# Kernel tuning notes

Measured on AMD Instinct MI355X. Metric: run time of the kernel, lower is better.

The kernel has to match this reference:

```python
import jax, jax.numpy as jnp
import numpy as np
from jax import lax

K = 8            # number of object slots
H = 250          # hidden / fc_size
EPS = 1e-5
DN = ('NCHW', 'OIHW', 'NCHW')


def ln_all(x):
    # F.layer_norm over all non-batch dims, no affine params (torch init: w=1,b=0)
    ax = tuple(range(1, x.ndim))
    m = jnp.mean(x, ax, keepdims=True)
    v = jnp.var(x, ax, keepdims=True)
    return (x - m) * lax.rsqrt(v + EPS)


def ln_last(x):
    # nn.LayerNorm(feat) -> last dim only
    m = jnp.mean(x, -1, keepdims=True)
    v = jnp.var(x, -1, keepdims=True)
    return (x - m) * lax.rsqrt(v + EPS)


def conv(x, w, b):
    # torch Conv2d(k=4, s=2, p=1), NCHW
    y = lax.conv_general_dilated(x, w, (2, 2), [(1, 1), (1, 1)], dimension_numbers=DN)
    return y + b[None, :, None, None]


def up4(x):
    return jnp.repeat(jnp.repeat(x, 4, axis=2), 4, axis=3)


def setup_inputs():
    ks = jax.random.split(jax.random.key(0), 20)
    bk = 48 * K
    p = lambda i, shape, s: jax.random.normal(ks[i], shape, jnp.float32) * s
    z = lambda n: jnp.zeros((n,), jnp.float32)
    return dict(
        x=p(0, (bk, 4096), 1.0),
        state=p(1, (bk, H), 1.0),
        # encoder convs (OIHW) + fc
        c1w=p(2, (16, 1, 4, 4), 0.25), c1b=z(16),
        c2w=p(3, (32, 16, 4, 4), 0.06), c2b=z(32),
        c3w=p(4, (64, 32, 4, 4), 0.04), c3b=z(64),
        efc_w=p(5, (4096, 512), 0.016), efc_b=z(512),
        # R_NEM (weights stored as [in, out])
        renc_w=p(6, (H, H), 0.06), renc_b=z(H),
        core_w=p(7, (2 * H, H), 0.045), core_b=z(H),
        ctx_w=p(8, (H, H), 0.06), ctx_b=z(H),
        att1_w=p(9, (H, 100), 0.06), att1_b=z(100),
        att2_w=p(10, (100, 1), 0.1), att2_b=z(1),
        out_w=p(11, (2 * H + 512, H), 0.03), out_b=z(H),
        # decoder fcs + convs
        dfc1_w=p(12, (H, 512), 0.06), dfc1_b=z(512),
        dfc2_w=p(13, (512, 4096), 0.045), dfc2_b=z(4096),
        d1w=p(14, (32, 64, 4, 4), 0.03), d1b=z(32),
        d2w=p(15, (16, 32, 4, 4), 0.045), d2b=z(16),
        d3w=p(16, (1, 16, 4, 4), 0.06), d3b=z(1),
    )


def reference(x, state, c1w, c1b, c2w, c2b, c3w, c3b, efc_w, efc_b,
              renc_w, renc_b, core_w, core_b, ctx_w, ctx_b,
              att1_w, att1_b, att2_w, att2_b, out_w, out_b,
              dfc1_w, dfc1_b, dfc2_w, dfc2_b, d1w, d1b, d2w, d2b, d3w, d3b):
    bk = x.shape[0]
    b = bk // K

    # ---------------- EncoderLayer ----------------
    def inwrap(h, w, bias):  # InputWrapper conv branch: NHWC -> permute(0,3,2,1) -> conv -> back
        y = conv(jnp.transpose(h, (0, 3, 2, 1)), w, bias)
        return jax.nn.elu(ln_all(jnp.transpose(y, (0, 3, 2, 1))))

    h = x.reshape(bk, 64, 64, 1)
    h = inwrap(h, c1w, c1b)                 # (bk,32,32,16)
    h = inwrap(h, c2w, c2b)                 # (bk,16,16,32)
    h = inwrap(h, c3w, c3b)                 # (bk,8,8,64)
    h = h.reshape(bk, -1)                   # (bk,4096)
    h = jax.nn.elu(ln_last(h @ efc_w + efc_b))   # (bk,512)

    # ---------------- R_NEM (RecurrentLayer) ----------------
    s1 = jax.nn.relu(ln_last(state @ renc_w + renc_b))   # (bk,H)
    s1r = s1.reshape(b, K, H)
    idx = np.array([[j for j in range(K) if j != i] for i in range(K)])  # (K,K-1)
    cs = s1r[:, idx, :]                                    # context: (b,K,K-1,H)
    fs = jnp.broadcast_to(s1r[:, :, None, :], cs.shape)    # focus copies
    pair = jnp.concatenate([fs, cs], axis=-1)              # (b,K,K-1,2H)
    core = jax.nn.relu(ln_last(pair @ core_w + core_b))    # (b,K,K-1,H)
    ctx = jax.nn.relu(ln_last(core @ ctx_w + ctx_b))       # (b,K,K-1,H)
    att = jax.nn.sigmoid(jnp.tanh(ln_last(core @ att1_w + att1_b)) @ att2_w + att2_b)  # (b,K,K-1,1)
    effect = jnp.sum(ctx * att, axis=2).reshape(bk, H)     # attention-weighted sum over K-1
    total = jnp.concatenate([s1, effect, h], axis=1)       # (bk, 2H+512)
    new_state = total @ out_w + out_b                      # (bk,H)
    xr = jax.nn.sigmoid(ln_last(new_state))
    state_out = jax.nn.sigmoid(new_state)

    # ---------------- DecoderLayer ----------------
    d = jax.nn.relu(ln_last(xr @ dfc1_w + dfc1_b))         # (bk,512)
    d = jax.nn.relu(ln_last(d @ dfc2_w + dfc2_b))          # (bk,4096)
    d = d.reshape(bk, 8, 8, 64)

    def outwrap(t, w, bias):
        y = conv(up4(jnp.transpose(t, (0, 3, 2, 1))), w, bias)
        return jnp.transpose(y, (0, 3, 2, 1))

    d = jax.nn.relu(ln_all(outwrap(d, d1w, d1b)))          # (bk,16,16,32)
    d = jax.nn.relu(ln_all(outwrap(d, d2w, d2b)))          # (bk,32,32,16)
    d = jax.nn.sigmoid(outwrap(d, d3w, d3b))               # (bk,64,64,1), no LN
    x_out = d.reshape(bk, -1)                              # (bk,4096)
    return x_out, state_out
```

## Files before the change

### kernel.cpp

```cpp
#include <hip/hip_runtime.h>
#include <hip/hip_bf16.h>
#include <math.h>

typedef __attribute__((ext_vector_type(8))) short bf16x8;
typedef __attribute__((ext_vector_type(4))) float f32x4;

__device__ __forceinline__ float eluf(float v){ return v > 0.f ? v : expm1f(v); }
__device__ __forceinline__ float sigf(float v){ return 1.f/(1.f+expf(-v)); }
__device__ __forceinline__ unsigned short f2bf(float f){
  unsigned u = __float_as_uint(f);
  u += 0x7FFFu + ((u >> 16) & 1u);
  return (unsigned short)(u >> 16);
}
__device__ __forceinline__ float bf2f(short s){
  return __uint_as_float(((unsigned)(unsigned short)s) << 16);
}

__device__ __forceinline__ void block_reduce2(float& a, float& b, float* sbuf){
  __syncthreads();
  for (int off = 32; off; off >>= 1){
    a += __shfl_down(a, off);
    b += __shfl_down(b, off);
  }
  int lane = threadIdx.x & 63, w = threadIdx.x >> 6;
  if (lane == 0){ sbuf[2*w] = a; sbuf[2*w+1] = b; }
  __syncthreads();
  if (threadIdx.x == 0){
    int nw = blockDim.x >> 6;
    float sa = 0.f, sb = 0.f;
    for (int i = 0; i < nw; i++){ sa += sbuf[2*i]; sb += sbuf[2*i+1]; }
    sbuf[0] = sa; sbuf[1] = sb;
  }
  __syncthreads();
  a = sbuf[0]; b = sbuf[1];
}

__device__ __forceinline__ float fold_sum(const float* __restrict__ w, int O, int I,
                                          int o, int i, int pa, int pb, int da, int db){
  float s = 0.f;
  for (int kh = 0; kh < 4; kh++){
    bool inh = (pb==0) ? (db==0 ? (kh==0) : (kh>=1)) : (db==0 ? (kh<=2) : (kh==3));
    if (!inh) continue;
    for (int kw = 0; kw < 4; kw++){
      bool inw = (pa==0) ? (da==0 ? (kw==0) : (kw>=1)) : (da==0 ? (kw<=2) : (kw==3));
      if (!inw) continue;
      s += w[((o*I + i)*4 + kh)*4 + kw];
    }
  }
  return s;
}
__device__ __forceinline__ void fold_elem(const float* __restrict__ w, float* __restrict__ CW,
                                          int O, int I, int l){
  int o = l % O; int q = l / O;
  int da = q & 1, db = (q>>1)&1, pa = (q>>2)&1, pb = (q>>3)&1, i = q>>4;
  CW[(((pb*2+pa)*4 + db*2+da)*I + i)*O + o] = fold_sum(w, O, I, o, i, pa, pb, da, db);
}
__device__ __forceinline__ void cvtc2_elem(const float* __restrict__ w, short* __restrict__ D, int l){
  int i = l & 15, t = (l>>4) & 15, o = l>>8;
  D[l] = (short)f2bf(w[(o*16 + i)*16 + t]);
}
__device__ __forceinline__ void cvtc3_elem(const float* __restrict__ w, short* __restrict__ D, int l){
  int i = l & 31, t = (l>>5) & 15, o = l>>9;
  D[l] = (short)f2bf(w[(o*32 + i)*16 + t]);
}
__device__ __forceinline__ void foldd1_elem(const float* __restrict__ w, short* __restrict__ D, int l){
  int i = l & 63, tap = (l>>6)&3, o = (l>>8)&31, ph = l>>13;
  D[l] = (short)f2bf(fold_sum(w, 32, 64, o, i, ph&1, ph>>1, tap&1, tap>>1));
}
__device__ __forceinline__ void foldd2_elem(const float* __restrict__ w, short* __restrict__ D, int l){
  int i = l & 31, tap = (l>>5)&3, o = (l>>7)&15, ph = l>>11;
  D[l] = (short)f2bf(fold_sum(w, 16, 32, o, i, ph&1, ph>>1, tap&1, tap>>1));
}

__global__ __launch_bounds__(256) void prep_combined(
  const float* __restrict__ efc,  short* __restrict__ Defc,
  const float* __restrict__ dfc2, short* __restrict__ Ddfc2,
  const float* __restrict__ outw, short* __restrict__ Dout,
  const float* __restrict__ corew,short* __restrict__ Dcore,
  const float* __restrict__ dfc1, short* __restrict__ Ddfc1,
  const float* __restrict__ renc, short* __restrict__ Drenc,
  const float* __restrict__ ctx,  short* __restrict__ Dctx,
  const float* __restrict__ att1, short* __restrict__ Datt1,
  const float* __restrict__ d3w, float* __restrict__ CWT3,
  const float* __restrict__ c2w, short* __restrict__ BtC2,
  const float* __restrict__ c3w, short* __restrict__ BtC3,
  const float* __restrict__ d1w, short* __restrict__ BD1,
  const float* __restrict__ d2w, short* __restrict__ BD2,
  const float* __restrict__ state, short* __restrict__ SBF,
  short* __restrict__ TOTb)
{
  int bx = blockIdx.x;
  if (bx >= 1192){
    const int F3=256, P2=F3+8192, P3=P2+32768, P4=P3+32768, P5=P4+8192,
              ST=P5+98304, TOTAL=ST+4608;
    for (int l = (bx-1192)*256 + threadIdx.x; l < TOTAL; l += 256*256){
      if (l < F3)      fold_elem(d3w, CWT3, 1, 16, l);
      else if (l < P2) cvtc2_elem(c2w, BtC2, l - F3);
      else if (l < P3) cvtc3_elem(c3w, BtC3, l - P2);
      else if (l < P4) foldd1_elem(d1w, BD1, l - P3);
      else if (l < P5) foldd2_elem(d2w, BD2, l - P4);
      else if (l < ST){
        int q = l - P5;
        int n = q >> 8, k = q & 255;
        SBF[q] = (k < 250) ? (short)f2bf(state[n*250 + k]) : (short)0;
      } else {
        int q = l - ST;
        int row = q / 12, cc = q % 12;
        int col = cc < 6 ? 250 + cc : 506 + (cc - 6);
        TOTb[row*1024 + col] = 0;
      }
    }
    return;
  }
  const float* W; short* D; int K, N, Kp, base, mode = 0;
  if      (bx < 512) { W=efc;  D=Defc;  K=4096; N=512;  Kp=4096; base=0;    }
  else if (bx < 1024){ W=dfc2; D=Ddfc2; K=512;  N=4096; Kp=512;  base=512;  }
  else if (bx < 1088){ W=outw; D=Dout;  K=1012; N=250;  Kp=1024; base=1024; mode=2; }
  else if (bx < 1120){ W=corew;D=Dcore; K=500;  N=250;  Kp=512;  base=1088; mode=1; }
  else if (bx < 1152){ W=dfc1; D=Ddfc1; K=250;  N=512;  Kp=256;  base=1120; }
  else if (bx < 1168){ W=renc; D=Drenc; K=250;  N=250;  Kp=256;  base=1152; }
  else if (bx < 1184){ W=ctx;  D=Dctx;  K=250;  N=250;  Kp=256;  base=1168; }
  else               { W=att1; D=Datt1; K=250;  N=100;  Kp=256;  base=1184; }
  int t = bx - base;
  int tpr = Kp >> 6;
  int tk = t % tpr, tn = t / tpr;
  __shared__ short tile[64][65];
  int c = threadIdx.x & 63, r4 = threadIdx.x >> 6;
  int n0 = tn*64, k0 = tk*64;
  #pragma unroll 4
  for (int p = 0; p < 16; p++){
    int r = r4*16 + p;
    int k = k0 + r, n = n0 + c;
    int ksrc = k; bool valid;
    if (mode == 0) valid = (k < K);
    else if (mode == 1){ valid = (k < 250) || (k >= 256 && k < 506); ksrc = k < 256 ? k : k - 6; }
    else { valid = (k < 250) || (k >= 256 && k < 506) || (k >= 512);
           ksrc = k < 256 ? k : (k < 512 ? k - 6 : k - 12); }
    float v = (valid && n < N) ? W[(size_t)ksrc*N + n] : 0.f;
    tile[c][r] = (short)f2bf(v);
  }
  __syncthreads();
  #pragma unroll 4
  for (int p = 0; p < 16; p++){
    int nn = r4*16 + p;
    int n = n0 + nn;
    if (n < N) D[(size_t)n*Kp + k0 + c] = tile[nn][c];
  }
}

__global__ __launch_bounds__(256) void gemm_mfma(
    const short* __restrict__ Ab, const short* __restrict__ Bt,
    float* __restrict__ P, int M, int N, int Kp, int Kc)
{
  __shared__ __align__(16) short As[64*32];
  __shared__ __align__(16) short Bs[64*32];
  int tid = threadIdx.x;
  int bm = blockIdx.y*64, bn = blockIdx.x*64;
  int kb = blockIdx.z * Kc;
  int kend = kb + Kc;

  int r = tid >> 2, c = tid & 3;
  const short* Arow = Ab + (size_t)(bm + r)*Kp;
  int gn = bn + r;
  bool bval = gn < N;
  const short* Brow = Bt + (size_t)gn*Kp;

  uint4 hA, hB;
  auto load_regs = [&](int k0){
    hA = *(const uint4*)&Arow[k0 + c*8];
    hB = bval ? *(const uint4*)&Brow[k0 + c*8] : make_uint4(0,0,0,0);
  };
  auto write_lds = [&](){
    *(uint4*)&As[r*32 + c*8] = hA;
    *(uint4*)&Bs[r*32 + c*8] = hB;
  };

  int wave = tid >> 6;
  int ln = tid & 15, quad = (tid >> 4) & 3;
  int wr = (wave >> 1) * 32, wc = (wave & 1) * 32;

  f32x4 zero = {0.f, 0.f, 0.f, 0.f};
  f32x4 acc[2][2] = {{zero, zero}, {zero, zero}};

  load_regs(kb);
  write_lds();
  __syncthreads();
  for (int k0 = kb; k0 < kend; k0 += 32){
    int nxt = k0 + 32;
    if (nxt < kend) load_regs(nxt);
    bf16x8 a0 = *(const bf16x8*)&As[(wr +      ln)*32 + quad*8];
    bf16x8 a1 = *(const bf16x8*)&As[(wr + 16 + ln)*32 + quad*8];
    bf16x8 b0 = *(const bf16x8*)&Bs[(wc +      ln)*32 + quad*8];
    bf16x8 b1 = *(const bf16x8*)&Bs[(wc + 16 + ln)*32 + quad*8];
    acc[0][0] = __builtin_amdgcn_mfma_f32_16x16x32_bf16(a0, b0, acc[0][0], 0, 0, 0);
    acc[0][1] = __builtin_amdgcn_mfma_f32_16x16x32_bf16(a0, b1, acc[0][1], 0, 0, 0);
    acc[1][0] = __builtin_amdgcn_mfma_f32_16x16x32_bf16(a1, b0, acc[1][0], 0, 0, 0);
    acc[1][1] = __builtin_amdgcn_mfma_f32_16x16x32_bf16(a1, b1, acc[1][1], 0, 0, 0);
    __syncthreads();
    if (nxt < kend){ write_lds(); __syncthreads(); }
  }

  float* Pout = P + (size_t)blockIdx.z*M*N;
  #pragma unroll
  for (int t = 0; t < 2; t++)
    #pragma unroll
    for (int u = 0; u < 2; u++)
      #pragma unroll
      for (int j = 0; j < 4; j++){
        int row = bm + wr + t*16 + quad*4 + j;
        int col = bn + wc + u*16 + ln;
        if (col < N) Pout[(size_t)row*N + col] = acc[t][u][j];
      }
}

__global__ __launch_bounds__(256) void gemm_conv2g(
    const short* __restrict__ In, const short* __restrict__ Bt,
    short* __restrict__ Out)
{
  __shared__ __align__(16) short As[128*32];
  __shared__ __align__(16) short Bs[32*32];
  int tid = threadIdx.x;
  int bm = blockIdx.x*128;

  int ra = tid >> 1, ca = (tid & 1)*16;
  int gr = bm + ra;
  int n = gr >> 8, pos = gr & 255;
  int oa = pos >> 4, ob = pos & 15;
  const short* ibase = In + (size_t)n*16384;
  int rb = tid >> 2, cb = (tid & 3)*8;
  const short* Brow = Bt + rb*256;
  bool bact = tid < 128;

  uint4 hA0, hA1, hB;
  auto load_regs = [&](int k0){
    #pragma unroll
    for (int h = 0; h < 2; h++){
      int k = k0 + ca + h*8;
      int tap = k >> 4;
      int ai = 2*oa + (tap & 3) - 1, bi = 2*ob + (tap >> 2) - 1;
      bool v = ((unsigned)ai < 32u) && ((unsigned)bi < 32u);
      uint4 tv = v ? *(const uint4*)&ibase[ai*512 + bi*16 + (k & 15)] : make_uint4(0,0,0,0);
      if (h == 0) hA0 = tv; else hA1 = tv;
    }
    if (bact) hB = *(const uint4*)&Brow[k0 + cb];
  };
  auto write_lds = [&](){
    *(uint4*)&As[ra*32 + ca] = hA0;
    *(uint4*)&As[ra*32 + ca + 8] = hA1;
    if (bact) *(uint4*)&Bs[rb*32 + cb] = hB;
  };

  int wave = tid >> 6, ln = tid & 15, quad = (tid >> 4) & 3;
  int wr = wave * 32;

  f32x4 zero = {0.f,0.f,0.f,0.f};
  f32x4 acc[2][2] = {{zero,zero},{zero,zero}};
  load_regs(0); write_lds(); __syncthreads();
  for (int k0 = 0; k0 < 256; k0 += 32){
    int nxt = k0 + 32;
    if (nxt < 256) load_regs(nxt);
    bf16x8 a0 = *(const bf16x8*)&As[(wr +      ln)*32 + quad*8];
    bf16x8 a1 = *(const bf16x8*)&As[(wr + 16 + ln)*32 + quad*8];
    bf16x8 b0 = *(const bf16x8*)&Bs[(     ln)*32 + quad*8];
    bf16x8 b1 = *(const bf16x8*)&Bs[(16 + ln)*32 + quad*8];
    acc[0][0] = __builtin_amdgcn_mfma_f32_16x16x32_bf16(a0, b0, acc[0][0], 0, 0, 0);
    acc[0][1] = __builtin_amdgcn_mfma_f32_16x16x32_bf16(a0, b1, acc[0][1], 0, 0, 0);
    acc[1][0] = __builtin_amdgcn_mfma_f32_16x16x32_bf16(a1, b0, acc[1][0], 0, 0, 0);
    acc[1][1] = __builtin_amdgcn_mfma_f32_16x16x32_bf16(a1, b1, acc[1][1], 0, 0, 0);
    __syncthreads();
    if (nxt < 256){ write_lds(); __syncthreads(); }
  }
  #pragma unroll
  for (int t = 0; t < 2; t++)
    #pragma unroll
    for (int u = 0; u < 2; u++)
      #pragma unroll
      for (int j = 0; j < 4; j++){
        int row = bm + wr + t*16 + quad*4 + j;
        int col = u*16 + ln;
        Out[(size_t)row*32 + col] = (short)f2bf(acc[t][u][j]);
      }
}

__global__ __launch_bounds__(256) void ln_conv2_act(
    short* __restrict__ E, const float* __restrict__ bias)
{
  __shared__ float sbuf[16];
  int n = blockIdx.x, tid = threadIdx.x;
  short* p = E + (size_t)n*8192;
  float vv[32];
  float s = 0.f, s2 = 0.f;
  #pragma unroll
  for (int t = 0; t < 4; t++){
    bf16x8 v8 = *(const bf16x8*)&p[(t*256 + tid)*8];
    #pragma unroll
    for (int j = 0; j < 8; j++){
      int i = (t*256 + tid)*8 + j;
      float v = bf2f(v8[j]) + bias[i & 31];
      vv[t*8+j] = v; s += v; s2 += v*v;
    }
  }
  block_reduce2(s, s2, sbuf);
  float m = s*(1.f/8192.f);
  float rs = rsqrtf(s2*(1.f/8192.f) - m*m + 1e-5f);
  #pragma unroll
  for (int t = 0; t < 4; t++){
    bf16x8 o8;
    #pragma unroll
    for (int j = 0; j < 8; j++)
      o8[j] = (short)f2bf(eluf((vv[t*8+j]-m)*rs));
    *(bf16x8*)&p[(t*256 + tid)*8] = o8;
  }
}

__global__ __launch_bounds__(256) void gemm_conv3g(
    const short* __restrict__ In, const short* __restrict__ Bt,
    float* __restrict__ P)
{
  __shared__ __align__(16) short As[64*32];
  __shared__ __align__(16) short Bs[64*32];
  int tid = threadIdx.x;
  int bm = blockIdx.x*64;

  int r = tid >> 2, c = tid & 3;
  int gr = bm + r;
  int n = gr >> 6, pos = gr & 63;
  int oa = pos >> 3, ob = pos & 7;
  const short* ibase = In + (size_t)n*8192;
  const short* Brow = Bt + r*512;

  uint4 hA, hB;
  auto load_regs = [&](int k0){
    int k = k0 + c*8;
    int tap = k >> 5;
    int ai = 2*oa + (tap & 3) - 1, bi = 2*ob + (tap >> 2) - 1;
    bool v = ((unsigned)ai < 16u) && ((unsigned)bi < 16u);
    hA = v ? *(const uint4*)&ibase[(ai*16 + bi)*32 + (k & 31)] : make_uint4(0,0,0,0);
    hB = *(const uint4*)&Brow[k];
  };
  auto write_lds = [&](){
    *(uint4*)&As[r*32 + c*8] = hA;
    *(uint4*)&Bs[r*32 + c*8] = hB;
  };

  int wave = tid >> 6, ln = tid & 15, quad = (tid >> 4) & 3;
  int wr = (wave >> 1) * 32, wc = (wave & 1) * 32;

  f32x4 zero = {0.f,0.f,0.f,0.f};
  f32x4 acc[2][2] = {{zero,zero},{zero,zero}};
  load_regs(0); write_lds(); __syncthreads();
  for (int k0 = 0; k0 < 512; k0 += 32){
    int nxt = k0 + 32;
    if (nxt < 512) load_regs(nxt);
    bf16x8 a0 = *(const bf16x8*)&As[(wr +      ln)*32 + quad*8];
    bf16x8 a1 = *(const bf16x8*)&As[(wr + 16 + ln)*32 + quad*8];
    bf16x8 b0 = *(const bf16x8*)&Bs[(wc +      ln)*32 + quad*8];
    bf16x8 b1 = *(const bf16x8*)&Bs[(wc + 16 + ln)*32 + quad*8];
    acc[0][0] = __builtin_amdgcn_mfma_f32_16x16x32_bf16(a0, b0, acc[0][0], 0, 0, 0);
    acc[0][1] = __builtin_amdgcn_mfma_f32_16x16x32_bf16(a0, b1, acc[0][1], 0, 0, 0);
    acc[1][0] = __builtin_amdgcn_mfma_f32_16x16x32_bf16(a1, b0, acc[1][0], 0, 0, 0);
    acc[1][1] = __builtin_amdgcn_mfma_f32_16x16x32_bf16(a1, b1, acc[1][1], 0, 0, 0);
    __syncthreads();
    if (nxt < 512){ write_lds(); __syncthreads(); }
  }
  #pragma unroll
  for (int t = 0; t < 2; t++)
    #pragma unroll
    for (int u = 0; u < 2; u++)
      #pragma unroll
      for (int j = 0; j < 4; j++){
        int row = bm + wr + t*16 + quad*4 + j;
        int col = wc + u*16 + ln;
        P[(size_t)row*64 + col] = acc[t][u][j];
      }
}

__global__ __launch_bounds__(256) void gemm_core_mfma(
    const short* __restrict__ Tb, const short* __restrict__ Bt,
    float* __restrict__ P, int M, int N, int Kc)
{
  __shared__ __align__(16) short As[64*32];
  __shared__ __align__(16) short Bs[64*32];
  int tid = threadIdx.x;
  int bm = blockIdx.y*64, bn = blockIdx.x*64;
  int kb = blockIdx.z * Kc;
  int kend = kb + Kc;

  int r = tid >> 2, c = tid & 3;
  int gr = bm + r;
  int jj2 = gr % 7, fi2 = gr / 7;
  int ii = fi2 & 7, j2 = fi2 >> 3;
  int jidx = jj2 < ii ? jj2 : jj2 + 1;
  const short* own = Tb + (size_t)fi2*1024;
  const short* oth = Tb + (size_t)(j2*8 + jidx)*1024;
  int gn = bn + r;
  bool bval = gn < N;
  const short* Brow = Bt + (size_t)gn*512;

  uint4 hA, hB;
  auto load_regs = [&](int k0){
    int kk = k0 + c*8;
    const short* src = (kk & 256) ? oth : own;
    hA = *(const uint4*)&src[kk & 255];
    hB = bval ? *(const uint4*)&Brow[kk] : make_uint4(0,0,0,0);
  };
  auto write_lds = [&](){
    *(uint4*)&As[r*32 + c*8] = hA;
    *(uint4*)&Bs[r*32 + c*8] = hB;
  };

  int wave = tid >> 6;
  int ln = tid & 15, quad = (tid >> 4) & 3;
  int wr = (wave >> 1) * 32, wc = (wave & 1) * 32;

  f32x4 zero = {0.f, 0.f, 0.f, 0.f};
  f32x4 acc[2][2] = {{zero, zero}, {zero, zero}};

  load_regs(kb);
  write_lds();
  __syncthreads();
  for (int k0 = kb; k0 < kend; k0 += 32){
    int nxt = k0 + 32;
    if (nxt < kend) load_regs(nxt);
    bf16x8 a0 = *(const bf16x8*)&As[(wr +      ln)*32 + quad*8];
    bf16x8 a1 = *(const bf16x8*)&As[(wr + 16 + ln)*32 + quad*8];
    bf16x8 b0 = *(const bf16x8*)&Bs[(wc +      ln)*32 + quad*8];
    bf16x8 b1 = *(const bf16x8*)&Bs[(wc + 16 + ln)*32 + quad*8];
    acc[0][0] = __builtin_amdgcn_mfma_f32_16x16x32_bf16(a0, b0, acc[0][0], 0, 0, 0);
    acc[0][1] = __builtin_amdgcn_mfma_f32_16x16x32_bf16(a0, b1, acc[0][1], 0, 0, 0);
    acc[1][0] = __builtin_amdgcn_mfma_f32_16x16x32_bf16(a1, b0, acc[1][0], 0, 0, 0);
    acc[1][1] = __builtin_amdgcn_mfma_f32_16x16x32_bf16(a1, b1, acc[1][1], 0, 0, 0);
    __syncthreads();
    if (nxt < kend){ write_lds(); __syncthreads(); }
  }

  float* Pout = P + (size_t)blockIdx.z*M*N;
  #pragma unroll
  for (int t = 0; t < 2; t++)
    #pragma unroll
    for (int u = 0; u < 2; u++)
      #pragma unroll
      for (int j = 0; j < 4; j++){
        int row = bm + wr + t*16 + quad*4 + j;
        int col = bn + wc + u*16 + ln;
        if (col < N) Pout[(size_t)row*N + col] = acc[t][u][j];
      }
}

__global__ __launch_bounds__(256) void reduce_ln(
    const float* __restrict__ Pp, const float* __restrict__ bias,
    void* __restrict__ outp, int M, int N, int KS, int os, int act, int obf, int bmask)
{
  __shared__ float rowbuf[4096];
  __shared__ float sbuf[16];
  int row = blockIdx.x;
  size_t MN = (size_t)M*N;
  float s = 0.f, s2 = 0.f;
  for (int c = threadIdx.x; c < N; c += 256){
    float v = bias[c & bmask];
    for (int ks = 0; ks < KS; ks++) v += Pp[ks*MN + (size_t)row*N + c];
    rowbuf[c] = v; s += v; s2 += v*v;
  }
  block_reduce2(s, s2, sbuf);
  float m = s / N;
  float r = rsqrtf(s2/N - m*m + 1e-5f);
  for (int c = threadIdx.x; c < N; c += 256){
    float v = (rowbuf[c]-m)*r;
    if (act == 1) v = fmaxf(v, 0.f);
    else if (act == 2) v = eluf(v);
    else if (act == 3) v = tanhf(v);
    if (obf) ((short*)outp)[(size_t)row*os + c] = f2bf(v);
    else     ((float*)outp)[(size_t)row*os + c] = v;
  }
}

__global__ __launch_bounds__(256) void reduce_ns(
    const float* __restrict__ Pp, const float* __restrict__ bias,
    short* __restrict__ XRb, float* __restrict__ so, int M, int N, int KS)
{
  __shared__ float rowbuf[256];
  __shared__ float sbuf[16];
  int row = blockIdx.x;
  size_t MN = (size_t)M*N;
  float s = 0.f, s2 = 0.f;
  for (int c = threadIdx.x; c < N; c += 256){
    float v = bias[c];
    for (int ks = 0; ks < KS; ks++) v += Pp[ks*MN + (size_t)row*N + c];
    rowbuf[c] = v; s += v; s2 += v*v;
  }
  block_reduce2(s, s2, sbuf);
  float m = s / N;
  float r = rsqrtf(s2/N - m*m + 1e-5f);
  for (int c = threadIdx.x; c < N; c += 256){
    float v = rowbuf[c];
    XRb[(size_t)row*256 + c] = f2bf(sigf((v-m)*r));
    so[(size_t)row*N + c] = sigf(v);
  }
}

__global__ __launch_bounds__(448) void ctx_att_effect(
    const float* __restrict__ Pc, const float* __restrict__ ctx_b,
    const float* __restrict__ Pa, const float* __restrict__ att1_b,
    const float* __restrict__ w2, const float* __restrict__ b2,
    short* __restrict__ tot)
{
  __shared__ float ctxs[7][250];
  __shared__ float att_s[7];
  int fi = blockIdx.x, tid = threadIdx.x;
  int jj = tid >> 6, lane = tid & 63;
  const size_t MN = (size_t)2688*250, MN2 = (size_t)2688*100;
  int row = fi*7 + jj;
  float vv[4];
  float s = 0.f, s2 = 0.f;
  #pragma unroll
  for (int t = 0; t < 4; t++){
    int c = lane + t*64;
    float v = 0.f;
    if (c < 250) v = ctx_b[c] + Pc[(size_t)row*250 + c] + Pc[MN + (size_t)row*250 + c];
    vv[t] = v; s += v; s2 += v*v;
  }
  #pragma unroll
  for (int off = 32; off; off >>= 1){ s += __shfl_down(s, off); s2 += __shfl_down(s2, off); }
  s = __shfl(s, 0); s2 = __shfl(s2, 0);
  float m = s*(1.f/250.f);
  float r = rsqrtf(s2*(1.f/250.f) - m*m + 1e-5f);
  #pragma unroll
  for (int t = 0; t < 4; t++){
    int c = lane + t*64;
    if (c < 250) ctxs[jj][c] = fmaxf((vv[t]-m)*r, 0.f);
  }
  float va[2];
  s = 0.f; s2 = 0.f;
  #pragma unroll
  for (int t = 0; t < 2; t++){
    int c = lane + t*64;
    float v = 0.f;
    if (c < 100){
      v = att1_b[c];
      #pragma unroll
      for (int ks = 0; ks < 4; ks++) v += Pa[ks*MN2 + (size_t)row*100 + c];
    }
    va[t] = v; s += v; s2 += v*v;
  }
  #pragma unroll
  for (int off = 32; off; off >>= 1){ s += __shfl_down(s, off); s2 += __shfl_down(s2, off); }
  s = __shfl(s, 0); s2 = __shfl(s2, 0);
  m = s*0.01f;
  r = rsqrtf(s2*0.01f - m*m + 1e-5f);
  float d = 0.f;
  #pragma unroll
  for (int t = 0; t < 2; t++){
    int c = lane + t*64;
    if (c < 100) d += tanhf((va[t]-m)*r)*w2[c];
  }
  #pragma unroll
  for (int off = 32; off; off >>= 1) d += __shfl_down(d, off);
  if (lane == 0) att_s[jj] = sigf(d + b2[0]);
  __syncthreads();
  for (int h = tid; h < 250; h += 448){
    float sum = 0.f;
    #pragma unroll
    for (int q = 0; q < 7; q++) sum += ctxs[q][h]*att_s[q];
    tot[(size_t)fi*1024 + 256 + h] = f2bf(sum);
  }
}

__global__ __launch_bounds__(256) void enc_conv1_ig(
    const float* __restrict__ x, const float* __restrict__ w, const float* __restrict__ bias,
    short* __restrict__ outp)
{
  __shared__ __align__(16) float in_t[66*68];
  __shared__ short rawb[16384];
  __shared__ float sbuf[16];
  int n = blockIdx.x, tid = threadIdx.x;
  for (int l = tid; l < 66*68; l += 256) in_t[l] = 0.f;
  __syncthreads();
  const float* xin = x + (size_t)n*4096;
  for (int l4 = tid; l4 < 1024; l4 += 256){
    float4 v = *(const float4*)&xin[l4*4];
    int aa = (l4*4) >> 6, bb = (l4*4) & 63;
    float* dst = &in_t[(aa+1)*68 + bb + 1];
    dst[0]=v.x; dst[1]=v.y; dst[2]=v.z; dst[3]=v.w;
  }
  int o = tid & 15;
  float wr[16];
  #pragma unroll
  for (int t = 0; t < 16; t++) wr[t] = w[o*16 + t];
  float bv = bias[o];
  __syncthreads();
  float s = 0.f, s2 = 0.f;
  for (int r = 0; r < 64; r++){
    int idx = tid + (r<<8);
    int bq = (idx>>4)&31, aq = idx>>9;
    int a0 = 2*aq, b0 = 2*bq;
    float acc = bv;
    #pragma unroll
    for (int kw = 0; kw < 4; kw++){
      const float* row = &in_t[(a0+kw)*68 + b0];
      float2 p0 = *(const float2*)&row[0];
      float2 p1 = *(const float2*)&row[2];
      acc += p0.x*wr[0*4+kw] + p0.y*wr[1*4+kw] + p1.x*wr[2*4+kw] + p1.y*wr[3*4+kw];
    }
    rawb[idx] = f2bf(acc);
    s += acc; s2 += acc*acc;
  }
  block_reduce2(s, s2, sbuf);
  float m = s*(1.f/16384.f);
  float rs = rsqrtf(s2*(1.f/16384.f) - m*m + 1e-5f);
  short* op = outp + (size_t)n*16384;
  for (int l = tid; l < 16384; l += 256){
    float v = bf2f(rawb[l]);
    op[l] = f2bf(eluf((v-m)*rs));
  }
}

__global__ __launch_bounds__(256) void dec_conv12_mfma(
    const short* __restrict__ in, const short* __restrict__ Bd1, const float* __restrict__ bias1,
    const short* __restrict__ Bd2, const float* __restrict__ bias2, short* __restrict__ outp)
{
  __shared__ __align__(16) short smem[18*18*32];
  __shared__ float sbuf[16];
  int n = blockIdx.x, tid = threadIdx.x;
  for (int l = tid; l < 1600; l += 256) ((unsigned long long*)smem)[l] = 0ull;
  __syncthreads();
  const short* ip = in + (size_t)n*4096;
  for (int l = tid; l < 1024; l += 256){
    int i4 = l & 15, sb = (l>>4)&7, sa = l>>7;
    *(uint2*)&smem[((sa+1)*10 + (sb+1))*64 + i4*4] = *(const uint2*)&ip[sa*512 + sb*64 + i4*4];
  }
  int wave = tid>>6, ln = tid&15, quad = (tid>>4)&3;
  int pa = wave & 1, pb = wave >> 1;
  bf16x8 bfr1[2][8];
  #pragma unroll
  for (int nt = 0; nt < 2; nt++){
    const short* Brow = Bd1 + (wave*32 + nt*16 + ln)*256;
    #pragma unroll
    for (int ks = 0; ks < 8; ks++)
      bfr1[nt][ks] = *(const bf16x8*)&Brow[ks*32 + quad*8];
  }
  __syncthreads();
  f32x4 z = {0.f,0.f,0.f,0.f};
  f32x4 acc[2][4] = {{z,z,z,z},{z,z,z,z}};
  #pragma unroll
  for (int ks = 0; ks < 8; ks++){
    int tap = ks>>1, ibase = (ks&1)*32 + quad*8;
    int da = tap & 1, db = tap >> 1;
    #pragma unroll
    for (int mt = 0; mt < 4; mt++){
      int p = mt*16 + ln;
      int ta = p>>3, tb = p&7;
      bf16x8 a = *(const bf16x8*)&smem[((ta+da+pa)*10 + (tb+db+pb))*64 + ibase];
      acc[0][mt] = __builtin_amdgcn_mfma_f32_16x16x32_bf16(a, bfr1[0][ks], acc[0][mt],0,0,0);
      acc[1][mt] = __builtin_amdgcn_mfma_f32_16x16x32_bf16(a, bfr1[1][ks], acc[1][mt],0,0,0);
    }
  }
  float s = 0.f, s2 = 0.f;
  #pragma unroll
  for (int nt = 0; nt < 2; nt++){
    float bz = bias1[nt*16 + ln];
    #pragma unroll
    for (int mt = 0; mt < 4; mt++)
      #pragma unroll
      for (int j = 0; j < 4; j++){
        float v = acc[nt][mt][j] + bz;
        acc[nt][mt][j] = v; s += v; s2 += v*v;
      }
  }
  block_reduce2(s, s2, sbuf);
  float m1 = s*(1.f/8192.f);
  float rs1 = rsqrtf(s2*(1.f/8192.f) - m1*m1 + 1e-5f);
  bf16x8 bfr2[4];
  {
    const short* Brow = Bd2 + (wave*16 + ln)*128;
    #pragma unroll
    for (int ks = 0; ks < 4; ks++)
      bfr2[ks] = *(const bf16x8*)&Brow[ks*32 + quad*8];
  }
  for (int l = tid; l < 2592; l += 256) ((unsigned long long*)smem)[l] = 0ull;
  __syncthreads();
  #pragma unroll
  for (int nt = 0; nt < 2; nt++){
    int o = nt*16 + ln;
    #pragma unroll
    for (int mt = 0; mt < 4; mt++)
      #pragma unroll
      for (int j = 0; j < 4; j++){
        int p = mt*16 + quad*4 + j;
        int ta = p>>3, tb = p&7;
        int sa = 2*ta + pa, sb = 2*tb + pb;
        smem[((sa+1)*18 + (sb+1))*32 + o] = f2bf(fmaxf((acc[nt][mt][j]-m1)*rs1, 0.f));
      }
  }
  __syncthreads();
  f32x4 acc2[16] = {z,z,z,z,z,z,z,z,z,z,z,z,z,z,z,z};
  #pragma unroll
  for (int ks = 0; ks < 4; ks++){
    int da = ks & 1, db = ks >> 1;
    #pragma unroll
    for (int mt = 0; mt < 16; mt++){
      int p = mt*16 + ln;
      int ta = p>>4, tb = p&15;
      bf16x8 a = *(const bf16x8*)&smem[((ta+da+pa)*18 + (tb+db+pb))*32 + quad*8];
      acc2[mt] = __builtin_amdgcn_mfma_f32_16x16x32_bf16(a, bfr2[ks], acc2[mt],0,0,0);
    }
  }
  s = 0.f; s2 = 0.f;
  float bz2 = bias2[ln];
  #pragma unroll
  for (int mt = 0; mt < 16; mt++)
    #pragma unroll
    for (int j = 0; j < 4; j++){
      float v = acc2[mt][j] + bz2;
      acc2[mt][j] = v; s += v; s2 += v*v;
    }
  block_reduce2(s, s2, sbuf);
  float m = s*(1.f/16384.f);
  float rs = rsqrtf(s2*(1.f/16384.f) - m*m + 1e-5f);
  short* op = outp + (size_t)n*16384;
  #pragma unroll
  for (int mt = 0; mt < 16; mt++)
    #pragma unroll
    for (int j = 0; j < 4; j++){
      int p = mt*16 + quad*4 + j;
      int ta = p>>4, tb = p&15;
      op[(2*ta+pa)*512 + (2*tb+pb)*16 + ln] = f2bf(fmaxf((acc2[mt][j]-m)*rs, 0.f));
    }
}

__global__ __launch_bounds__(256) void dec_conv3_ig(
    const short* __restrict__ in, const float* __restrict__ CWT, const float* __restrict__ bias,
    float* __restrict__ outp)
{
  __shared__ __align__(16) float in_t[9792];
  __shared__ __align__(16) float wl[256];
  int bx = blockIdx.x;
  int n = bx >> 1, b0 = (bx & 1) * 32, tb0 = b0 >> 1;
  int tid = threadIdx.x;
  const short* ip = in + (size_t)n*16384;
  for (int l = tid; l < 9792; l += 256){
    int i = l & 15, sb = (l >> 4) % 18, sap = l / 288;
    int sa = sap - 1, sbg = tb0 - 1 + sb;
    float v = 0.f;
    if ((unsigned)sa < 32u && (unsigned)sbg < 32u)
      v = bf2f(ip[sa*512 + sbg*16 + i]);
    in_t[(sap*18 + sb)*16 + i] = v;
  }
  for (int l = tid; l < 256; l += 256) wl[l] = CWT[l];
  __syncthreads();
  float bv = bias[0];
  int bl = tid & 31, ath = tid >> 5;
  int b = b0 + bl;
  int tb = b >> 1, pb = b & 1;
  float* op = outp + (size_t)n*4096;
  #pragma unroll
  for (int j = 0; j < 8; j++){
    int a = ath*8 + j;
    int ta = a >> 1, pa = a & 1;
    float4 s4 = make_float4(0.f,0.f,0.f,0.f);
    #pragma unroll
    for (int db = 0; db < 2; db++){
      int sb = tb + db + (pb ? 0 : -1);
      int sbl = sb - (tb0 - 1);
      #pragma unroll
      for (int da = 0; da < 2; da++){
        int sa = ta + da + (pa ? 0 : -1);
        int sap = sa + 1;
        const float4* A4 = (const float4*)&in_t[(sap*18 + sbl)*16];
        const float4* B4 = (const float4*)&wl[((pb*2+pa)*4 + db*2+da)*16];
        #pragma unroll
        for (int q = 0; q < 4; q++){
          float4 av = A4[q], bw = B4[q];
          s4.x += av.x*bw.x; s4.y += av.y*bw.y;
          s4.z += av.z*bw.z; s4.w += av.w*bw.w;
        }
      }
    }
    op[a*64 + b] = sigf(bv + s4.x + s4.y + s4.z + s4.w);
  }
}

extern "C" void kernel_launch(void* const* d_in, const int* in_sizes, int n_in,
                              void* d_out, int out_size, void* d_ws, size_t ws_size,
                              hipStream_t stream) {
  const float* x      = (const float*)d_in[0];
  const float* state  = (const float*)d_in[1];
  const float* c1w    = (const float*)d_in[2];
  const float* c1b    = (const float*)d_in[3];
  const float* c2w    = (const float*)d_in[4];
  const float* c2b    = (const float*)d_in[5];
  const float* c3w    = (const float*)d_in[6];
  const float* c3b    = (const float*)d_in[7];
  const float* efc_w  = (const float*)d_in[8];
  const float* efc_b  = (const float*)d_in[9];
  const float* renc_w = (const float*)d_in[10];
  const float* renc_b = (const float*)d_in[11];
  const float* core_w = (const float*)d_in[12];
  const float* core_b = (const float*)d_in[13];
  const float* ctx_w  = (const float*)d_in[14];
  const float* ctx_b  = (const float*)d_in[15];
  const float* att1_w = (const float*)d_in[16];
  const float* att1_b = (const float*)d_in[17];
  const float* att2_w = (const float*)d_in[18];
  const float* att2_b = (const float*)d_in[19];
  const float* out_w  = (const float*)d_in[20];
  const float* out_b  = (const float*)d_in[21];
  const float* dfc1_w = (const float*)d_in[22];
  const float* dfc1_b = (const float*)d_in[23];
  const float* dfc2_w = (const float*)d_in[24];
  const float* dfc2_b = (const float*)d_in[25];
  const float* d1w    = (const float*)d_in[26];
  const float* d1b    = (const float*)d_in[27];
  const float* d2w    = (const float*)d_in[28];
  const float* d2b    = (const float*)d_in[29];
  const float* d3w    = (const float*)d_in[30];
  const float* d3b    = (const float*)d_in[31];

  float* wsf = (float*)d_ws;
  size_t o = 0;
  float* PB   = wsf + o; o += (size_t)1600*1024;
  float* PB2  = wsf + o; o += (size_t)2688*100*4;
  float* CWT3 = wsf + o; o += 256;
  short* E1b  = (short*)(wsf + o); o += (size_t)384*16384/2;
  short* E2b  = (short*)(wsf + o); o += (size_t)384*8192/2;
  short* E3b  = (short*)(wsf + o); o += (size_t)384*4096/2;
  short* TOTb = (short*)(wsf + o); o += (size_t)384*1024/2;
  short* C1b  = (short*)(wsf + o); o += (size_t)2688*256/2;
  short* XRb  = (short*)(wsf + o); o += (size_t)384*256/2;
  short* G1b  = (short*)(wsf + o); o += (size_t)384*512/2;
  short* SBF  = (short*)(wsf + o); o += (size_t)384*256/2;
  short* BtC2 = (short*)(wsf + o); o += 8192/2;
  short* BtC3 = (short*)(wsf + o); o += 32768/2;
  short* BD1  = (short*)(wsf + o); o += 32768/2;
  short* BD2  = (short*)(wsf + o); o += 8192/2;
  short* BT_efc  = (short*)(wsf + o); o += 2097152/2;
  short* BT_renc = (short*)(wsf + o); o += 64000/2;
  short* BT_core = (short*)(wsf + o); o += 128000/2;
  short* BT_ctx  = (short*)(wsf + o); o += 64000/2;
  short* BT_att1 = (short*)(wsf + o); o += 25600/2;
  short* BT_out  = (short*)(wsf + o); o += 256000/2;
  short* BT_dfc1 = (short*)(wsf + o); o += 131072/2;
  short* BT_dfc2 = (short*)(wsf + o); o += 2097152/2;
  short* D2b = E1b;
  short* G2b = E3b;

  float* xout = (float*)d_out;
  float* sout = xout + (size_t)384*4096;

  prep_combined<<<1448, 256, 0, stream>>>(
      efc_w, BT_efc, dfc2_w, BT_dfc2, out_w, BT_out, core_w, BT_core,
      dfc1_w, BT_dfc1, renc_w, BT_renc, ctx_w, BT_ctx, att1_w, BT_att1,
      d3w, CWT3, c2w, BtC2, c3w, BtC3, d1w, BD1, d2w, BD2, state, SBF, TOTb);

  enc_conv1_ig<<<384, 256, 0, stream>>>(x, c1w, c1b, E1b);
  gemm_conv2g<<<768, 256, 0, stream>>>(E1b, BtC2, E2b);
  ln_conv2_act<<<384, 256, 0, stream>>>(E2b, c2b);
  gemm_conv3g<<<384, 256, 0, stream>>>(E2b, BtC3, PB);
  reduce_ln<<<384, 256, 0, stream>>>(PB, c3b, E3b, 384, 4096, 1, 4096, 2, 1, 63);
  gemm_mfma<<<dim3(8,6,8), 256, 0, stream>>>(E3b, BT_efc, PB, 384, 512, 4096, 512);
  reduce_ln<<<384, 256, 0, stream>>>(PB, efc_b, TOTb+512, 384, 512, 8, 1024, 2, 1, -1);

  gemm_mfma<<<dim3(4,6,8), 256, 0, stream>>>(SBF, BT_renc, PB, 384, 250, 256, 32);
  reduce_ln<<<384, 256, 0, stream>>>(PB, renc_b, TOTb, 384, 250, 8, 1024, 1, 1, -1);
  gemm_core_mfma<<<dim3(4,42,2), 256, 0, stream>>>(TOTb, BT_core, PB, 2688, 250, 256);
  reduce_ln<<<2688, 256, 0, stream>>>(PB, core_b, C1b, 2688, 250, 2, 256, 1, 1, -1);
  gemm_mfma<<<dim3(4,42,2), 256, 0, stream>>>(C1b, BT_ctx, PB, 2688, 250, 256, 128);
  gemm_mfma<<<dim3(2,42,4), 256, 0, stream>>>(C1b, BT_att1, PB2, 2688, 100, 256, 64);
  ctx_att_effect<<<384, 448, 0, stream>>>(PB, ctx_b, PB2, att1_b, att2_w, att2_b, TOTb);

  gemm_mfma<<<dim3(4,6,8), 256, 0, stream>>>(TOTb, BT_out, PB, 384, 250, 1024, 128);
  reduce_ns<<<384, 256, 0, stream>>>(PB, out_b, XRb, sout, 384, 250, 8);

  gemm_mfma<<<dim3(8,6,4), 256, 0, stream>>>(XRb, BT_dfc1, PB, 384, 512, 256, 64);
  reduce_ln<<<384, 256, 0, stream>>>(PB, dfc1_b, G1b, 384, 512, 4, 512, 1, 1, -1);
  gemm_mfma<<<dim3(64,6,1), 256, 0, stream>>>(G1b, BT_dfc2, PB, 384, 4096, 512, 512);
  reduce_ln<<<384, 256, 0, stream>>>(PB, dfc2_b, G2b, 384, 4096, 1, 4096, 1, 1, -1);

  dec_conv12_mfma<<<384, 256, 0, stream>>>(G2b, BD1, d1b, BD2, d2b, D2b);
  dec_conv3_ig<<<768, 256, 0, stream>>>(D2b, CWT3, d3b, xout);

  (void)in_sizes; (void)n_in; (void)out_size; (void)ws_size;
}
```

Before: 339.7 us.

## Fuse encoder conv2 LN, conv3 GEMM and LN into one kernel; merge ctx/att1 GEMMs

Replaces the conv2 layer-norm kernel, the conv3 implicit GEMM and its reduce_ln with a single per-sample kernel. It normalizes conv2 output into a padded LDS image, runs conv3 with MFMA, and applies LN+ELU in registers. It also concatenates the ctx and att1 weights into one padded B matrix so a single GEMM replaces two launches, and widens the decoder LDS row stride from 32/64 to 40/72 to avoid bank conflicts. This removes launches and fp32 partial round-trips, but conv3 now runs with only 384 blocks doing all 16 K-steps each, and the att half of the merged GEMM does padded work.

```diff
diff --git a/kernel.cpp b/kernel.cpp
--- a/kernel.cpp
+++ b/kernel.cpp
@@ -79,8 +79,8 @@
   const float* __restrict__ corew,short* __restrict__ Dcore,
   const float* __restrict__ dfc1, short* __restrict__ Ddfc1,
   const float* __restrict__ renc, short* __restrict__ Drenc,
-  const float* __restrict__ ctx,  short* __restrict__ Dctx,
-  const float* __restrict__ att1, short* __restrict__ Datt1,
+  const float* __restrict__ ctx,  const float* __restrict__ att1,
+  short* __restrict__ Dctxatt,
   const float* __restrict__ d3w, float* __restrict__ CWT3,
   const float* __restrict__ c2w, short* __restrict__ BtC2,
   const float* __restrict__ c3w, short* __restrict__ BtC3,
@@ -92,7 +92,7 @@
   int bx = blockIdx.x;
   if (bx >= 1192){
     const int F3=256, P2=F3+8192, P3=P2+32768, P4=P3+32768, P5=P4+8192,
-              ST=P5+98304, TOTAL=ST+4608;
+              ST=P5+98304, TP=ST+4608, TOTAL=TP+8704;
     for (int l = (bx-1192)*256 + threadIdx.x; l < TOTAL; l += 256*256){
       if (l < F3)      fold_elem(d3w, CWT3, 1, 16, l);
       else if (l < P2) cvtc2_elem(c2w, BtC2, l - F3);
@@ -103,11 +103,16 @@
         int q = l - P5;
         int n = q >> 8, k = q & 255;
         SBF[q] = (k < 250) ? (short)f2bf(state[n*250 + k]) : (short)0;
-      } else {
+      } else if (l < TP){
         int q = l - ST;
         int row = q / 12, cc = q % 12;
         int col = cc < 6 ? 250 + cc : 506 + (cc - 6);
         TOTb[row*1024 + col] = 0;
+      } else {
+        int q = l - TP;
+        int r = q >> 8, cc = q & 255;
+        int row = r < 6 ? 250 + r : 356 + (r - 6);
+        Dctxatt[row*256 + cc] = 0;
       }
     }
     return;
@@ -119,8 +124,8 @@
   else if (bx < 1120){ W=corew;D=Dcore; K=500;  N=250;  Kp=512;  base=1088; mode=1; }
   else if (bx < 1152){ W=dfc1; D=Ddfc1; K=250;  N=512;  Kp=256;  base=1120; }
   else if (bx < 1168){ W=renc; D=Drenc; K=250;  N=250;  Kp=256;  base=1152; }
-  else if (bx < 1184){ W=ctx;  D=Dctx;  K=250;  N=250;  Kp=256;  base=1168; }
-  else               { W=att1; D=Datt1; K=250;  N=100;  Kp=256;  base=1184; }
+  else if (bx < 1184){ W=ctx;  D=Dctxatt;         K=250; N=250; Kp=256; base=1168; }
+  else               { W=att1; D=Dctxatt + 65536; K=250; N=100; Kp=256; base=1184; }
   int t = bx - base;
   int tpr = Kp >> 6;
   int tk = t % tpr, tn = t / tpr;
@@ -282,97 +287,87 @@
       }
 }
 
-__global__ __launch_bounds__(256) void ln_conv2_act(
-    short* __restrict__ E, const float* __restrict__ bias)
-{
+__global__ __launch_bounds__(256) void enc_conv3_full(
+    const short* __restrict__ E2raw, const float* __restrict__ bias2,
+    const short* __restrict__ Bt3, const float* __restrict__ bias3,
+    short* __restrict__ outp)
+{
+  __shared__ __align__(16) short lsamp[18*18*40];
   __shared__ float sbuf[16];
   int n = blockIdx.x, tid = threadIdx.x;
-  short* p = E + (size_t)n*8192;
+  const short* ip = E2raw + (size_t)n*8192;
   float vv[32];
   float s = 0.f, s2 = 0.f;
   #pragma unroll
   for (int t = 0; t < 4; t++){
-    bf16x8 v8 = *(const bf16x8*)&p[(t*256 + tid)*8];
+    bf16x8 v8 = *(const bf16x8*)&ip[(t*256 + tid)*8];
     #pragma unroll
     for (int j = 0; j < 8; j++){
-      int i = (t*256 + tid)*8 + j;
-      float v = bf2f(v8[j]) + bias[i & 31];
+      int e = (t*256 + tid)*8 + j;
+      float v = bf2f(v8[j]) + bias2[e & 31];
       vv[t*8+j] = v; s += v; s2 += v*v;
     }
   }
   block_reduce2(s, s2, sbuf);
-  float m = s*(1.f/8192.f);
-  float rs = rsqrtf(s2*(1.f/8192.f) - m*m + 1e-5f);
+  float m2 = s*(1.f/8192.f);
+  float rs2 = rsqrtf(s2*(1.f/8192.f) - m2*m2 + 1e-5f);
+  for (int l = tid; l < 18*18*40/4; l += 256) ((unsigned long long*)lsamp)[l] = 0ull;
+  __syncthreads();
   #pragma unroll
   for (int t = 0; t < 4; t++){
+    int e0 = (t*256 + tid)*8;
+    int slot = e0 >> 5, ch0 = e0 & 31;
+    int a = slot >> 4, b = slot & 15;
     bf16x8 o8;
     #pragma unroll
     for (int j = 0; j < 8; j++)
-      o8[j] = (short)f2bf(eluf((vv[t*8+j]-m)*rs));
-    *(bf16x8*)&p[(t*256 + tid)*8] = o8;
-  }
-}
-
-__global__ __launch_bounds__(256) void gemm_conv3g(
-    const short* __restrict__ In, const short* __restrict__ Bt,
-    float* __restrict__ P)
-{
-  __shared__ __align__(16) short As[64*32];
-  __shared__ __align__(16) short Bs[64*32];
-  int tid = threadIdx.x;
-  int bm = blockIdx.x*64;
-
-  int r = tid >> 2, c = tid & 3;
-  int gr = bm + r;
-  int n = gr >> 6, pos = gr & 63;
-  int oa = pos >> 3, ob = pos & 7;
-  const short* ibase = In + (size_t)n*8192;
-  const short* Brow = Bt + r*512;
-
-  uint4 hA, hB;
-  auto load_regs = [&](int k0){
-    int k = k0 + c*8;
-    int tap = k >> 5;
-    int ai = 2*oa + (tap & 3) - 1, bi = 2*ob + (tap >> 2) - 1;
-    bool v = ((unsigned)ai < 16u) && ((unsigned)bi < 16u);
-    hA = v ? *(const uint4*)&ibase[(ai*16 + bi)*32 + (k & 31)] : make_uint4(0,0,0,0);
-    hB = *(const uint4*)&Brow[k];
-  };
-  auto write_lds = [&](){
-    *(uint4*)&As[r*32 + c*8] = hA;
-    *(uint4*)&Bs[r*32 + c*8] = hB;
-  };
-
-  int wave = tid >> 6, ln = tid & 15, quad = (tid >> 4) & 3;
-  int wr = (wave >> 1) * 32, wc = (wave & 1) * 32;
-
-  f32x4 zero = {0.f,0.f,0.f,0.f};
-  f32x4 acc[2][2] = {{zero,zero},{zero,zero}};
-  load_regs(0); write_lds(); __syncthreads();
-  for (int k0 = 0; k0 < 512; k0 += 32){
-    int nxt = k0 + 32;
-    if (nxt < 512) load_regs(nxt);
-    bf16x8 a0 = *(const bf16x8*)&As[(wr +      ln)*32 + quad*8];
-    bf16x8 a1 = *(const bf16x8*)&As[(wr + 16 + ln)*32 + quad*8];
-    bf16x8 b0 = *(const bf16x8*)&Bs[(wc +      ln)*32 + quad*8];
-    bf16x8 b1 = *(const bf16x8*)&Bs[(wc + 16 + ln)*32 + quad*8];
-    acc[0][0] = __builtin_amdgcn_mfma_f32_16x16x32_bf16(a0, b0, acc[0][0], 0, 0, 0);
-    acc[0][1] = __builtin_amdgcn_mfma_f32_16x16x32_bf16(a0, b1, acc[0][1], 0, 0, 0);
-    acc[1][0] = __builtin_amdgcn_mfma_f32_16x16x32_bf16(a1, b0, acc[1][0], 0, 0, 0);
-    acc[1][1] = __builtin_amdgcn_mfma_f32_16x16x32_bf16(a1, b1, acc[1][1], 0, 0, 0);
-    __syncthreads();
-    if (nxt < 512){ write_lds(); __syncthreads(); }
-  }
-  #pragma unroll
-  for (int t = 0; t < 2; t++)
-    #pragma unroll
-    for (int u = 0; u < 2; u++)
-      #pragma unroll
-      for (int j = 0; j < 4; j++){
-        int row = bm + wr + t*16 + quad*4 + j;
-        int col = wc + u*16 + ln;
-        P[(size_t)row*64 + col] = acc[t][u][j];
-      }
+      o8[j] = (short)f2bf(eluf((vv[t*8+j]-m2)*rs2));
+    *(bf16x8*)&lsamp[((a+1)*18 + (b+1))*40 + ch0] = o8;
+  }
+  int wave = tid>>6, ln = tid&15, quad = (tid>>4)&3;
+  int o3 = wave*16 + ln;
+  bf16x8 bfr3[16];
+  {
+    const short* Brow = Bt3 + o3*512;
+    #pragma unroll
+    for (int ks = 0; ks < 16; ks++)
+      bfr3[ks] = *(const bf16x8*)&Brow[ks*32 + quad*8];
+  }
+  __syncthreads();
+  f32x4 z = {0.f,0.f,0.f,0.f};
+  f32x4 acc3[4] = {z,z,z,z};
+  #pragma unroll
+  for (int ks = 0; ks < 16; ks++){
+    int kh = ks>>2, kw = ks&3;
+    #pragma unroll
+    for (int mt = 0; mt < 4; mt++){
+      int p = mt*16 + ln;
+      int oa = p>>3, ob = p&7;
+      bf16x8 a = *(const bf16x8*)&lsamp[((2*oa+kw)*18 + (2*ob+kh))*40 + quad*8];
+      acc3[mt] = __builtin_amdgcn_mfma_f32_16x16x32_bf16(a, bfr3[ks], acc3[mt],0,0,0);
+    }
+  }
+  s = 0.f; s2 = 0.f;
+  float bz3 = bias3[o3];
+  #pragma unroll
+  for (int mt = 0; mt < 4; mt++)
+    #pragma unroll
+    for (int j = 0; j < 4; j++){
+      float v = acc3[mt][j] + bz3;
+      acc3[mt][j] = v; s += v; s2 += v*v;
+    }
+  block_reduce2(s, s2, sbuf);
+  float m3 = s*(1.f/4096.f);
+  float rs3 = rsqrtf(s2*(1.f/4096.f) - m3*m3 + 1e-5f);
+  short* op = outp + (size_t)n*4096;
+  #pragma unroll
+  for (int mt = 0; mt < 4; mt++)
+    #pragma unroll
+    for (int j = 0; j < 4; j++){
+      int p = mt*16 + quad*4 + j;
+      int oa = p>>3, ob = p&7;
+      op[oa*512 + ob*64 + o3] = f2bf(eluf((acc3[mt][j]-m3)*rs3));
+    }
 }
 
 __global__ __launch_bounds__(256) void gemm_core_mfma(
@@ -500,7 +495,7 @@
 
 __global__ __launch_bounds__(448) void ctx_att_effect(
     const float* __restrict__ Pc, const float* __restrict__ ctx_b,
-    const float* __restrict__ Pa, const float* __restrict__ att1_b,
+    const float* __restrict__ att1_b,
     const float* __restrict__ w2, const float* __restrict__ b2,
     short* __restrict__ tot)
 {
@@ -508,7 +503,7 @@
   __shared__ float att_s[7];
   int fi = blockIdx.x, tid = threadIdx.x;
   int jj = tid >> 6, lane = tid & 63;
-  const size_t MN = (size_t)2688*250, MN2 = (size_t)2688*100;
+  const size_t MN = (size_t)2688*384;
   int row = fi*7 + jj;
   float vv[4];
   float s = 0.f, s2 = 0.f;
@@ -516,7 +511,7 @@
   for (int t = 0; t < 4; t++){
     int c = lane + t*64;
     float v = 0.f;
-    if (c < 250) v = ctx_b[c] + Pc[(size_t)row*250 + c] + Pc[MN + (size_t)row*250 + c];
+    if (c < 250) v = ctx_b[c] + Pc[(size_t)row*384 + c] + Pc[MN + (size_t)row*384 + c];
     vv[t] = v; s += v; s2 += v*v;
   }
   #pragma unroll
@@ -535,11 +530,8 @@
   for (int t = 0; t < 2; t++){
     int c = lane + t*64;
     float v = 0.f;
-    if (c < 100){
-      v = att1_b[c];
-      #pragma unroll
-      for (int ks = 0; ks < 4; ks++) v += Pa[ks*MN2 + (size_t)row*100 + c];
-    }
+    if (c < 100)
+      v = att1_b[c] + Pc[(size_t)row*384 + 256 + c] + Pc[MN + (size_t)row*384 + 256 + c];
     va[t] = v; s += v; s2 += v*v;
   }
   #pragma unroll
@@ -618,15 +610,15 @@
     const short* __restrict__ in, const short* __restrict__ Bd1, const float* __restrict__ bias1,
     const short* __restrict__ Bd2, const float* __restrict__ bias2, short* __restrict__ outp)
 {
-  __shared__ __align__(16) short smem[18*18*32];
+  __shared__ __align__(16) short smem[18*18*40];
   __shared__ float sbuf[16];
   int n = blockIdx.x, tid = threadIdx.x;
-  for (int l = tid; l < 1600; l += 256) ((unsigned long long*)smem)[l] = 0ull;
+  for (int l = tid; l < 1800; l += 256) ((unsigned long long*)smem)[l] = 0ull;
   __syncthreads();
   const short* ip = in + (size_t)n*4096;
   for (int l = tid; l < 1024; l += 256){
     int i4 = l & 15, sb = (l>>4)&7, sa = l>>7;
-    *(uint2*)&smem[((sa+1)*10 + (sb+1))*64 + i4*4] = *(const uint2*)&ip[sa*512 + sb*64 + i4*4];
+    *(uint2*)&smem[((sa+1)*10 + (sb+1))*72 + i4*4] = *(const uint2*)&ip[sa*512 + sb*64 + i4*4];
   }
   int wave = tid>>6, ln = tid&15, quad = (tid>>4)&3;
   int pa = wave & 1, pb = wave >> 1;
@@ -649,7 +641,7 @@
     for (int mt = 0; mt < 4; mt++){
       int p = mt*16 + ln;
       int ta = p>>3, tb = p&7;
-      bf16x8 a = *(const bf16x8*)&smem[((ta+da+pa)*10 + (tb+db+pb))*64 + ibase];
+      bf16x8 a = *(const bf16x8*)&smem[((ta+da+pa)*10 + (tb+db+pb))*72 + ibase];
       acc[0][mt] = __builtin_amdgcn_mfma_f32_16x16x32_bf16(a, bfr1[0][ks], acc[0][mt],0,0,0);
       acc[1][mt] = __builtin_amdgcn_mfma_f32_16x16x32_bf16(a, bfr1[1][ks], acc[1][mt],0,0,0);
     }
@@ -676,7 +668,7 @@
     for (int ks = 0; ks < 4; ks++)
       bfr2[ks] = *(const bf16x8*)&Brow[ks*32 + quad*8];
   }
-  for (int l = tid; l < 2592; l += 256) ((unsigned long long*)smem)[l] = 0ull;
+  for (int l = tid; l < 3240; l += 256) ((unsigned long long*)smem)[l] = 0ull;
   __syncthreads();
   #pragma unroll
   for (int nt = 0; nt < 2; nt++){
@@ -688,7 +680,7 @@
         int p = mt*16 + quad*4 + j;
         int ta = p>>3, tb = p&7;
         int sa = 2*ta + pa, sb = 2*tb + pb;
-        smem[((sa+1)*18 + (sb+1))*32 + o] = f2bf(fmaxf((acc[nt][mt][j]-m1)*rs1, 0.f));
+        smem[((sa+1)*18 + (sb+1))*40 + o] = f2bf(fmaxf((acc[nt][mt][j]-m1)*rs1, 0.f));
       }
   }
   __syncthreads();
@@ -700,7 +692,7 @@
     for (int mt = 0; mt < 16; mt++){
       int p = mt*16 + ln;
       int ta = p>>4, tb = p&15;
-      bf16x8 a = *(const bf16x8*)&smem[((ta+da+pa)*18 + (tb+db+pb))*32 + quad*8];
+      bf16x8 a = *(const bf16x8*)&smem[((ta+da+pa)*18 + (tb+db+pb))*40 + quad*8];
       acc2[mt] = __builtin_amdgcn_mfma_f32_16x16x32_bf16(a, bfr2[ks], acc2[mt],0,0,0);
     }
   }
@@ -817,8 +809,7 @@
 
   float* wsf = (float*)d_ws;
   size_t o = 0;
-  float* PB   = wsf + o; o += (size_t)1600*1024;
-  float* PB2  = wsf + o; o += (size_t)2688*100*4;
+  float* PB   = wsf + o; o += (size_t)2112*1024;
   float* CWT3 = wsf + o; o += 256;
   short* E1b  = (short*)(wsf + o); o += (size_t)384*16384/2;
   short* E2b  = (short*)(wsf + o); o += (size_t)384*8192/2;
@@ -832,14 +823,13 @@
   short* BtC3 = (short*)(wsf + o); o += 32768/2;
   short* BD1  = (short*)(wsf + o); o += 32768/2;
   short* BD2  = (short*)(wsf + o); o += 8192/2;
-  short* BT_efc  = (short*)(wsf + o); o += 2097152/2;
-  short* BT_renc = (short*)(wsf + o); o += 64000/2;
-  short* BT_core = (short*)(wsf + o); o += 128000/2;
-  short* BT_ctx  = (short*)(wsf + o); o += 64000/2;
-  short* BT_att1 = (short*)(wsf + o); o += 25600/2;
-  short* BT_out  = (short*)(wsf + o); o += 256000/2;
-  short* BT_dfc1 = (short*)(wsf + o); o += 131072/2;
-  short* BT_dfc2 = (short*)(wsf + o); o += 2097152/2;
+  short* BT_efc    = (short*)(wsf + o); o += 2097152/2;
+  short* BT_renc   = (short*)(wsf + o); o += 64000/2;
+  short* BT_core   = (short*)(wsf + o); o += 128000/2;
+  short* BT_ctxatt = (short*)(wsf + o); o += 98304/2;
+  short* BT_out    = (short*)(wsf + o); o += 256000/2;
+  short* BT_dfc1   = (short*)(wsf + o); o += 131072/2;
+  short* BT_dfc2   = (short*)(wsf + o); o += 2097152/2;
   short* D2b = E1b;
   short* G2b = E3b;
 
@@ -848,14 +838,12 @@
 
   prep_combined<<<1448, 256, 0, stream>>>(
       efc_w, BT_efc, dfc2_w, BT_dfc2, out_w, BT_out, core_w, BT_core,
-      dfc1_w, BT_dfc1, renc_w, BT_renc, ctx_w, BT_ctx, att1_w, BT_att1,
+      dfc1_w, BT_dfc1, renc_w, BT_renc, ctx_w, att1_w, BT_ctxatt,
       d3w, CWT3, c2w, BtC2, c3w, BtC3, d1w, BD1, d2w, BD2, state, SBF, TOTb);
 
   enc_conv1_ig<<<384, 256, 0, stream>>>(x, c1w, c1b, E1b);
   gemm_conv2g<<<768, 256, 0, stream>>>(E1b, BtC2, E2b);
-  ln_conv2_act<<<384, 256, 0, stream>>>(E2b, c2b);
-  gemm_conv3g<<<384, 256, 0, stream>>>(E2b, BtC3, PB);
-  reduce_ln<<<384, 256, 0, stream>>>(PB, c3b, E3b, 384, 4096, 1, 4096, 2, 1, 63);
+  enc_conv3_full<<<384, 256, 0, stream>>>(E2b, c2b, BtC3, c3b, E3b);
   gemm_mfma<<<dim3(8,6,8), 256, 0, stream>>>(E3b, BT_efc, PB, 384, 512, 4096, 512);
   reduce_ln<<<384, 256, 0, stream>>>(PB, efc_b, TOTb+512, 384, 512, 8, 1024, 2, 1, -1);
 
@@ -863,9 +851,8 @@
   reduce_ln<<<384, 256, 0, stream>>>(PB, renc_b, TOTb, 384, 250, 8, 1024, 1, 1, -1);
   gemm_core_mfma<<<dim3(4,42,2), 256, 0, stream>>>(TOTb, BT_core, PB, 2688, 250, 256);
   reduce_ln<<<2688, 256, 0, stream>>>(PB, core_b, C1b, 2688, 250, 2, 256, 1, 1, -1);
-  gemm_mfma<<<dim3(4,42,2), 256, 0, stream>>>(C1b, BT_ctx, PB, 2688, 250, 256, 128);
-  gemm_mfma<<<dim3(2,42,4), 256, 0, stream>>>(C1b, BT_att1, PB2, 2688, 100, 256, 64);
-  ctx_att_effect<<<384, 448, 0, stream>>>(PB, ctx_b, PB2, att1_b, att2_w, att2_b, TOTb);
+  gemm_mfma<<<dim3(6,42,2), 256, 0, stream>>>(C1b, BT_ctxatt, PB, 2688, 384, 256, 128);
+  ctx_att_effect<<<384, 448, 0, stream>>>(PB, ctx_b, att1_b, att2_w, att2_b, TOTb);
 
   gemm_mfma<<<dim3(4,6,8), 256, 0, stream>>>(TOTb, BT_out, PB, 384, 250, 1024, 128);
   reduce_ns<<<384, 256, 0, stream>>>(PB, out_b, XRb, sout, 384, 250, 8);
```

New measurement: 322.3 us. 5.1% less time.
